# Performance work log

Hardware: AMD Instinct MI355X
Metric: run time of the kernel (lower is better)

The kernel has to match this reference:

```python
import jax, jax.numpy as jnp
import numpy as np

N = 1_048_576      # flattened batch (forward reshapes to (-1, 4))
Q_DIM = 4
HIDDEN = 64
DC = Q_DIM // 2    # q_dim_changed = 2
NUM_LO = (DC * DC - DC) // 2  # = 1
SLOPE = 0.01       # torch leaky_relu default negative slope


def setup_inputs() -> dict:
    key = jax.random.key(0)
    ks = jax.random.split(key, 9)
    def lin(kw, kb, fan_out, fan_in):
        bound = 1.0 / np.sqrt(fan_in)
        W = jax.random.uniform(kw, (fan_out, fan_in), jnp.float32, -bound, bound)
        b = jax.random.uniform(kb, (fan_out,), jnp.float32, -bound, bound)
        return W, b
    x = jax.random.normal(ks[0], (N, Q_DIM), jnp.float32)
    W1, b1 = lin(ks[1], ks[2], HIDDEN, Q_DIM)
    W2, b2 = lin(ks[3], ks[4], HIDDEN, HIDDEN)
    W_Ld, b_Ld = lin(ks[5], ks[6], DC, HIDDEN)
    W_Lo, b_Lo = lin(ks[7], ks[8], NUM_LO, HIDDEN)
    return {"x": x, "W1": W1, "b1": b1, "W2": W2, "b2": b2,
            "W_Ld": W_Ld, "b_Ld": b_Ld, "W_Lo": W_Lo, "b_Lo": b_Lo}


def reference(x, W1, b1, W2, b2, W_Ld, b_Ld, W_Lo, b_Lo):
    q = x.reshape(-1, Q_DIM)                      # (n, 4)
    n = q.shape[0]
    h1 = jax.nn.leaky_relu(q @ W1.T + b1, SLOPE)  # (n, 64)
    h2 = jax.nn.leaky_relu(h1 @ W2.T + b2, SLOPE) # (n, 64); dropout is eval-mode identity
    Ld = jax.nn.softplus(h2 @ W_Ld.T + b_Ld)      # (n, 2) positive diagonal
    Lo = h2 @ W_Lo.T + b_Lo                       # (n, 1) strictly-lower entries
    rows, cols = jnp.tril_indices(DC, -1)         # strictly lower triangle, row-major
    diag = jnp.arange(DC)
    L = jnp.zeros((n, DC, DC), dtype=q.dtype)
    L = L.at[:, rows, cols].set(Lo)               # scatter Lo (matches torch boolean-mask fill order)
    L = L.at[:, diag, diag].set(Ld)               # diag_embed(Ld)
    H = jnp.einsum('nij,nkj->nik', L, L) + 1e-9 * jnp.eye(DC, dtype=q.dtype)
    return H
```

## Files before the change

kernel.cpp:

```cpp
#include <hip/hip_runtime.h>


typedef __attribute__((ext_vector_type(8))) short bf16x8;
typedef __attribute__((ext_vector_type(4))) float f32x4;
typedef __attribute__((ext_vector_type(2))) float f32x2;

#define BLOCK_THREADS  256
#define GRID_BLOCKS    1280
#define ROWS_PER_GROUP 256

__device__ __forceinline__ float lrelu(float a) {
    return fmaxf(a, 0.01f * a);
}

__device__ __forceinline__ f32x2 lrelu2(f32x2 a) {
    return __builtin_elementwise_max(a, a * 0.01f);
}

__device__ __forceinline__ float softplus(float v) {
    return fmaxf(v, 0.0f) + log1pf(expf(-fabsf(v)));
}

__device__ __forceinline__ unsigned cvt_pk_bf16(float lo, float hi) {
    unsigned r;
    asm("v_cvt_pk_bf16_f32 %0, %1, %2" : "=v"(r) : "v"(lo), "v"(hi));
    return r;
}

__device__ __forceinline__ float lo_of(float v, unsigned pk, bool hi_half) {
    const float h = __uint_as_float(hi_half ? (pk & 0xFFFF0000u) : (pk << 16));
    return v - h;
}

__global__ __launch_bounds__(BLOCK_THREADS) void dln_mfma(
    const float* __restrict__ x,
    const float* __restrict__ W1,  const float* __restrict__ b1,
    const float* __restrict__ W2,  const float* __restrict__ b2,
    const float* __restrict__ WLd, const float* __restrict__ bLd,
    const float* __restrict__ WLo, const float* __restrict__ bLo,
    float* __restrict__ out, int ngroups)
{
    __shared__ __align__(16) unsigned short h1s[4][8][64][8];

    const int tid  = threadIdx.x;
    const int lane = tid & 63;
    const int wv   = tid >> 6;
    const int quad = lane >> 4;
    const int c    = lane & 15;

    int grp = blockIdx.x;
    float4 qnext = ((const float4*)x)[grp * ROWS_PER_GROUP + tid];

    bf16x8 afrag[4][2];
    f32x4 b2v[4];
#pragma unroll
    for (int mt = 0; mt < 4; ++mt) {
        const int nu = 32 * (mt >> 1) + 8 * (c >> 2) + 4 * (mt & 1) + (c & 3);
        const float* wr = W2 + nu * 64 + 8 * quad;
#pragma unroll
        for (int s = 0; s < 2; ++s) {
            const float4 f0 = *(const float4*)(wr + 32 * s);
            const float4 f1 = *(const float4*)(wr + 32 * s + 4);
            uint4 u;
            u.x = cvt_pk_bf16(f0.x, f0.y);
            u.y = cvt_pk_bf16(f0.z, f0.w);
            u.z = cvt_pk_bf16(f1.x, f1.y);
            u.w = cvt_pk_bf16(f1.z, f1.w);
            afrag[mt][s] = __builtin_bit_cast(bf16x8, u);
        }
        b2v[mt] = *(const f32x4*)(b2 + 32 * (mt >> 1) + 4 * (mt & 1) + 8 * quad);
    }

    bf16x8 hA[2][2];
    {
        const float* hw = (c == 0) ? WLd : (c == 1) ? (WLd + 64) : WLo;
#pragma unroll
        for (int s = 0; s < 2; ++s) {
            uint4 uh = make_uint4(0u, 0u, 0u, 0u);
            uint4 ul = make_uint4(0u, 0u, 0u, 0u);
            if (c < 3) {
                const float* p = hw + 32 * s + 8 * quad;
                const float4 f0 = *(const float4*)(p);
                const float4 f1 = *(const float4*)(p + 4);
                uh.x = cvt_pk_bf16(f0.x, f0.y);
                uh.y = cvt_pk_bf16(f0.z, f0.w);
                uh.z = cvt_pk_bf16(f1.x, f1.y);
                uh.w = cvt_pk_bf16(f1.z, f1.w);
                ul.x = cvt_pk_bf16(lo_of(f0.x, uh.x, false), lo_of(f0.y, uh.x, true));
                ul.y = cvt_pk_bf16(lo_of(f0.z, uh.y, false), lo_of(f0.w, uh.y, true));
                ul.z = cvt_pk_bf16(lo_of(f1.x, uh.z, false), lo_of(f1.y, uh.z, true));
                ul.w = cvt_pk_bf16(lo_of(f1.z, uh.w, false), lo_of(f1.w, uh.w, true));
            }
            hA[s][0] = __builtin_bit_cast(bf16x8, uh);
            hA[s][1] = __builtin_bit_cast(bf16x8, ul);
        }
    }
    const float bld0 = bLd[0];
    const float bld1 = bLd[1];
    const float blo0 = bLo[0];
    const f32x4 hinit = (quad == 0) ? (f32x4){bld0, bld1, blo0, 0.0f}
                                    : (f32x4){0.0f, 0.0f, 0.0f, 0.0f};

    for (; grp < ngroups; grp += (int)gridDim.x) {
        const float4 qv = qnext;
        const int gn = grp + (int)gridDim.x;
        if (gn < ngroups)
            qnext = ((const float4*)x)[gn * ROWS_PER_GROUP + tid];
        const int wbase = grp * ROWS_PER_GROUP + wv * 64;

#pragma unroll
        for (int ch = 0; ch < 8; ++ch) {
            unsigned up[4];
#pragma unroll
            for (int p = 0; p < 4; ++p) {
                float h[2];
#pragma unroll
                for (int e = 0; e < 2; ++e) {
                    const int j = ch * 8 + p * 2 + e;
                    float a = b1[j];
                    a = fmaf(qv.x, W1[4 * j + 0], a);
                    a = fmaf(qv.y, W1[4 * j + 1], a);
                    a = fmaf(qv.z, W1[4 * j + 2], a);
                    a = fmaf(qv.w, W1[4 * j + 3], a);
                    h[e] = lrelu(a);
                }
                up[p] = cvt_pk_bf16(h[0], h[1]);
            }
            *(uint4*)&h1s[wv][ch][lane][0] = make_uint4(up[0], up[1], up[2], up[3]);
        }

#pragma unroll
        for (int it = 0; it < 4; ++it) {
            const bf16x8 bf0 = *(const bf16x8*)&h1s[wv][quad][it * 16 + c][0];
            const bf16x8 bf1 = *(const bf16x8*)&h1s[wv][4 + quad][it * 16 + c][0];

            uint4 u0, u1;
#pragma unroll
            for (int mt = 0; mt < 4; ++mt) {
                f32x4 acc = b2v[mt];
                acc = __builtin_amdgcn_mfma_f32_16x16x32_bf16(afrag[mt][0], bf0, acc, 0, 0, 0);
                acc = __builtin_amdgcn_mfma_f32_16x16x32_bf16(afrag[mt][1], bf1, acc, 0, 0, 0);
                const f32x2 hlo = lrelu2((f32x2){acc[0], acc[1]});
                const f32x2 hhi = lrelu2((f32x2){acc[2], acc[3]});
                const unsigned pa = cvt_pk_bf16(hlo[0], hlo[1]);
                const unsigned pb = cvt_pk_bf16(hhi[0], hhi[1]);
                if (mt == 0)      { u0.x = pa; u0.y = pb; }
                else if (mt == 1) { u0.z = pa; u0.w = pb; }
                else if (mt == 2) { u1.x = pa; u1.y = pb; }
                else              { u1.z = pa; u1.w = pb; }
            }
            const bf16x8 bh0 = __builtin_bit_cast(bf16x8, u0);
            const bf16x8 bh1 = __builtin_bit_cast(bf16x8, u1);

            f32x4 hacc = hinit;
            hacc = __builtin_amdgcn_mfma_f32_16x16x32_bf16(hA[0][0], bh0, hacc, 0, 0, 0);
            hacc = __builtin_amdgcn_mfma_f32_16x16x32_bf16(hA[0][1], bh0, hacc, 0, 0, 0);
            hacc = __builtin_amdgcn_mfma_f32_16x16x32_bf16(hA[1][0], bh1, hacc, 0, 0, 0);
            hacc = __builtin_amdgcn_mfma_f32_16x16x32_bf16(hA[1][1], bh1, hacc, 0, 0, 0);

            if (quad == 0) {
                const float ld0 = softplus(hacc[0]);
                const float ld1 = softplus(hacc[1]);
                const float lo  = hacc[2];
                float4 o;
                o.x = fmaf(ld0, ld0, 1e-9f);
                o.y = ld0 * lo;
                o.z = o.y;
                o.w = fmaf(lo, lo, fmaf(ld1, ld1, 1e-9f));
                reinterpret_cast<float4*>(out)[wbase + it * 16 + c] = o;
            }
        }
    }
}

__global__ __launch_bounds__(256) void dln_tail(
    const float* __restrict__ x,
    const float* __restrict__ W1,  const float* __restrict__ b1,
    const float* __restrict__ W2,  const float* __restrict__ b2,
    const float* __restrict__ WLd, const float* __restrict__ bLd,
    const float* __restrict__ WLo, const float* __restrict__ bLo,
    float* __restrict__ out, int row0, int nrows)
{
    const int row = row0 + blockIdx.x * 256 + threadIdx.x;
    if (row >= nrows) return;
    const float4 qv = reinterpret_cast<const float4*>(x)[row];
    float h1[64];
#pragma unroll
    for (int j = 0; j < 64; ++j) {
        float a = b1[j];
        a = fmaf(qv.x, W1[4 * j + 0], a);
        a = fmaf(qv.y, W1[4 * j + 1], a);
        a = fmaf(qv.z, W1[4 * j + 2], a);
        a = fmaf(qv.w, W1[4 * j + 3], a);
        h1[j] = lrelu(a);
    }
    float ld0 = bLd[0], ld1 = bLd[1], lo = bLo[0];
#pragma unroll 4
    for (int j = 0; j < 64; ++j) {
        float a0 = b2[j], a1 = 0.0f;
        const float* w = W2 + 64 * j;
#pragma unroll
        for (int k = 0; k < 64; k += 2) {
            a0 = fmaf(h1[k],     w[k],     a0);
            a1 = fmaf(h1[k + 1], w[k + 1], a1);
        }
        const float a = lrelu(a0 + a1);
        ld0 = fmaf(a, WLd[j],      ld0);
        ld1 = fmaf(a, WLd[64 + j], ld1);
        lo  = fmaf(a, WLo[j],      lo);
    }
    ld0 = softplus(ld0);
    ld1 = softplus(ld1);
    float4 o;
    o.x = fmaf(ld0, ld0, 1e-9f);
    o.y = ld0 * lo;
    o.z = o.y;
    o.w = fmaf(lo, lo, fmaf(ld1, ld1, 1e-9f));
    reinterpret_cast<float4*>(out)[row] = o;
}

extern "C" void kernel_launch(void* const* d_in, const int* in_sizes, int n_in,
                              void* d_out, int out_size, void* d_ws, size_t ws_size,
                              hipStream_t stream)
{
    const float* x   = (const float*)d_in[0];
    const float* W1  = (const float*)d_in[1];
    const float* b1  = (const float*)d_in[2];
    const float* W2  = (const float*)d_in[3];
    const float* b2  = (const float*)d_in[4];
    const float* WLd = (const float*)d_in[5];
    const float* bLd = (const float*)d_in[6];
    const float* WLo = (const float*)d_in[7];
    const float* bLo = (const float*)d_in[8];
    float* out = (float*)d_out;

    const int nrows   = in_sizes[0] / 4;
    const int ngroups = nrows / ROWS_PER_GROUP;
    const int nfull   = ngroups * ROWS_PER_GROUP;
    const int rem     = nrows - nfull;

    if (ngroups > 0) {
        const int grid = (ngroups < GRID_BLOCKS) ? ngroups : GRID_BLOCKS;
        dln_mfma<<<grid, BLOCK_THREADS, 0, stream>>>(
            x, W1, b1, W2, b2, WLd, bLd, WLo, bLo, out, ngroups);
    }
    if (rem > 0)
        dln_tail<<<(rem + 255) / 256, 256, 0, stream>>>(
            x, W1, b1, W2, b2, WLd, bLd, WLo, bLo, out, nfull, nrows);
}
```

Before: 137.5 us.

## Compute first layer with MFMA and drop shared-memory staging and persistent loop

Moves the 4->64 first layer from per-thread scalar FMAs (staged through LDS) onto a bf16 MFMA, using hi/lo bf16 splitting of W1 and x plus a ones column to fold in the bias. The first-layer result stays in registers as the B operand of the second-layer MFMA, so the LDS buffer is removed. The persistent grid-stride loop with x prefetch is replaced by one block per 256-row group, and the final head accumulates into two independent accumulators to shorten the MFMA dependency chain. Per-block setup (weight fragment conversion) now repeats for every group instead of being amortized across a persistent block, and bf16 precision of the first layer changes slightly.

After: 147.5 us. 7.3% more time.

```diff
diff --git a/kernel.cpp b/kernel.cpp
--- a/kernel.cpp
+++ b/kernel.cpp
@@ -6,7 +6,6 @@
 typedef __attribute__((ext_vector_type(2))) float f32x2;
 
 #define BLOCK_THREADS  256
-#define GRID_BLOCKS    1280
 #define ROWS_PER_GROUP 256
 
 __device__ __forceinline__ float lrelu(float a) {
@@ -38,18 +37,42 @@
     const float* __restrict__ W2,  const float* __restrict__ b2,
     const float* __restrict__ WLd, const float* __restrict__ bLd,
     const float* __restrict__ WLo, const float* __restrict__ bLo,
-    float* __restrict__ out, int ngroups)
+    float* __restrict__ out)
 {
-    __shared__ __align__(16) unsigned short h1s[4][8][64][8];
-
     const int tid  = threadIdx.x;
     const int lane = tid & 63;
     const int wv   = tid >> 6;
     const int quad = lane >> 4;
     const int c    = lane & 15;
 
-    int grp = blockIdx.x;
-    float4 qnext = ((const float4*)x)[grp * ROWS_PER_GROUP + tid];
+    const int wbase = blockIdx.x * ROWS_PER_GROUP + wv * 64;
+
+    float4 xv[4];
+#pragma unroll
+    for (int it = 0; it < 4; ++it)
+        xv[it] = ((const float4*)x)[wbase + it * 16 + c];
+
+    bf16x8 a1[4];
+#pragma unroll
+    for (int mt = 0; mt < 4; ++mt) {
+        const int nu = 32 * (mt >> 1) + 8 * (c >> 2) + 4 * (mt & 1) + (c & 3);
+        const float4 w = *(const float4*)(W1 + 4 * nu);
+        const float bb = b1[nu];
+        const unsigned h01 = cvt_pk_bf16(w.x, w.y);
+        const unsigned h23 = cvt_pk_bf16(w.z, w.w);
+        uint4 u = make_uint4(0u, 0u, 0u, 0u);
+        if (quad == 0) {
+            const unsigned t = cvt_pk_bf16(bb, 0.0f);
+            const float bl = bb - __uint_as_float(t << 16);
+            u.x = h01; u.y = h23;
+            u.z = cvt_pk_bf16(bb, bl);
+        } else if (quad == 1) {
+            u.x = cvt_pk_bf16(lo_of(w.x, h01, false), lo_of(w.y, h01, true));
+            u.y = cvt_pk_bf16(lo_of(w.z, h23, false), lo_of(w.w, h23, true));
+            u.z = h01; u.w = h23;
+        }
+        a1[mt] = __builtin_bit_cast(bf16x8, u);
+    }
 
     bf16x8 afrag[4][2];
     f32x4 b2v[4];
@@ -95,80 +118,87 @@
             hA[s][1] = __builtin_bit_cast(bf16x8, ul);
         }
     }
-    const float bld0 = bLd[0];
-    const float bld1 = bLd[1];
-    const float blo0 = bLo[0];
-    const f32x4 hinit = (quad == 0) ? (f32x4){bld0, bld1, blo0, 0.0f}
-                                    : (f32x4){0.0f, 0.0f, 0.0f, 0.0f};
-
-    for (; grp < ngroups; grp += (int)gridDim.x) {
-        const float4 qv = qnext;
-        const int gn = grp + (int)gridDim.x;
-        if (gn < ngroups)
-            qnext = ((const float4*)x)[gn * ROWS_PER_GROUP + tid];
-        const int wbase = grp * ROWS_PER_GROUP + wv * 64;
-
-#pragma unroll
-        for (int ch = 0; ch < 8; ++ch) {
-            unsigned up[4];
-#pragma unroll
-            for (int p = 0; p < 4; ++p) {
-                float h[2];
-#pragma unroll
-                for (int e = 0; e < 2; ++e) {
-                    const int j = ch * 8 + p * 2 + e;
-                    float a = b1[j];
-                    a = fmaf(qv.x, W1[4 * j + 0], a);
-                    a = fmaf(qv.y, W1[4 * j + 1], a);
-                    a = fmaf(qv.z, W1[4 * j + 2], a);
-                    a = fmaf(qv.w, W1[4 * j + 3], a);
-                    h[e] = lrelu(a);
-                }
-                up[p] = cvt_pk_bf16(h[0], h[1]);
-            }
-            *(uint4*)&h1s[wv][ch][lane][0] = make_uint4(up[0], up[1], up[2], up[3]);
-        }
-
-#pragma unroll
-        for (int it = 0; it < 4; ++it) {
-            const bf16x8 bf0 = *(const bf16x8*)&h1s[wv][quad][it * 16 + c][0];
-            const bf16x8 bf1 = *(const bf16x8*)&h1s[wv][4 + quad][it * 16 + c][0];
-
-            uint4 u0, u1;
-#pragma unroll
-            for (int mt = 0; mt < 4; ++mt) {
-                f32x4 acc = b2v[mt];
-                acc = __builtin_amdgcn_mfma_f32_16x16x32_bf16(afrag[mt][0], bf0, acc, 0, 0, 0);
-                acc = __builtin_amdgcn_mfma_f32_16x16x32_bf16(afrag[mt][1], bf1, acc, 0, 0, 0);
-                const f32x2 hlo = lrelu2((f32x2){acc[0], acc[1]});
-                const f32x2 hhi = lrelu2((f32x2){acc[2], acc[3]});
-                const unsigned pa = cvt_pk_bf16(hlo[0], hlo[1]);
-                const unsigned pb = cvt_pk_bf16(hhi[0], hhi[1]);
-                if (mt == 0)      { u0.x = pa; u0.y = pb; }
-                else if (mt == 1) { u0.z = pa; u0.w = pb; }
-                else if (mt == 2) { u1.x = pa; u1.y = pb; }
-                else              { u1.z = pa; u1.w = pb; }
-            }
-            const bf16x8 bh0 = __builtin_bit_cast(bf16x8, u0);
-            const bf16x8 bh1 = __builtin_bit_cast(bf16x8, u1);
-
-            f32x4 hacc = hinit;
-            hacc = __builtin_amdgcn_mfma_f32_16x16x32_bf16(hA[0][0], bh0, hacc, 0, 0, 0);
-            hacc = __builtin_amdgcn_mfma_f32_16x16x32_bf16(hA[0][1], bh0, hacc, 0, 0, 0);
-            hacc = __builtin_amdgcn_mfma_f32_16x16x32_bf16(hA[1][0], bh1, hacc, 0, 0, 0);
-            hacc = __builtin_amdgcn_mfma_f32_16x16x32_bf16(hA[1][1], bh1, hacc, 0, 0, 0);
-
-            if (quad == 0) {
-                const float ld0 = softplus(hacc[0]);
-                const float ld1 = softplus(hacc[1]);
-                const float lo  = hacc[2];
-                float4 o;
-                o.x = fmaf(ld0, ld0, 1e-9f);
-                o.y = ld0 * lo;
-                o.z = o.y;
-                o.w = fmaf(lo, lo, fmaf(ld1, ld1, 1e-9f));
-                reinterpret_cast<float4*>(out)[wbase + it * 16 + c] = o;
-            }
+    const f32x4 hinit = (quad == 0)
+        ? (f32x4){bLd[0], bLd[1], bLo[0], 0.0f}
+        : (f32x4){0.0f, 0.0f, 0.0f, 0.0f};
+
+#pragma unroll
+    for (int it = 0; it < 4; ++it) {
+        const unsigned xh01 = cvt_pk_bf16(xv[it].x, xv[it].y);
+        const unsigned xh23 = cvt_pk_bf16(xv[it].z, xv[it].w);
+        uint4 ub = make_uint4(0u, 0u, 0u, 0u);
+        if (quad == 0) {
+            ub.x = xh01; ub.y = xh23; ub.z = 0x3F803F80u;
+        } else if (quad == 1) {
+            ub.x = xh01; ub.y = xh23;
+            ub.z = cvt_pk_bf16(lo_of(xv[it].x, xh01, false), lo_of(xv[it].y, xh01, true));
+            ub.w = cvt_pk_bf16(lo_of(xv[it].z, xh23, false), lo_of(xv[it].w, xh23, true));
+        }
+        const bf16x8 bx = __builtin_bit_cast(bf16x8, ub);
+
+        f32x4 acc1[4];
+#pragma unroll
+        for (int mt = 0; mt < 4; ++mt)
+            acc1[mt] = __builtin_amdgcn_mfma_f32_16x16x32_bf16(
+                a1[mt], bx, (f32x4){0.0f, 0.0f, 0.0f, 0.0f}, 0, 0, 0);
+
+        uint4 u0, u1;
+        {
+            const f32x2 p0 = lrelu2((f32x2){acc1[0][0], acc1[0][1]});
+            const f32x2 p1 = lrelu2((f32x2){acc1[0][2], acc1[0][3]});
+            const f32x2 p2 = lrelu2((f32x2){acc1[1][0], acc1[1][1]});
+            const f32x2 p3 = lrelu2((f32x2){acc1[1][2], acc1[1][3]});
+            const f32x2 p4 = lrelu2((f32x2){acc1[2][0], acc1[2][1]});
+            const f32x2 p5 = lrelu2((f32x2){acc1[2][2], acc1[2][3]});
+            const f32x2 p6 = lrelu2((f32x2){acc1[3][0], acc1[3][1]});
+            const f32x2 p7 = lrelu2((f32x2){acc1[3][2], acc1[3][3]});
+            u0.x = cvt_pk_bf16(p0[0], p0[1]);
+            u0.y = cvt_pk_bf16(p1[0], p1[1]);
+            u0.z = cvt_pk_bf16(p2[0], p2[1]);
+            u0.w = cvt_pk_bf16(p3[0], p3[1]);
+            u1.x = cvt_pk_bf16(p4[0], p4[1]);
+            u1.y = cvt_pk_bf16(p5[0], p5[1]);
+            u1.z = cvt_pk_bf16(p6[0], p6[1]);
+            u1.w = cvt_pk_bf16(p7[0], p7[1]);
+        }
+        const bf16x8 bf0 = __builtin_bit_cast(bf16x8, u0);
+        const bf16x8 bf1 = __builtin_bit_cast(bf16x8, u1);
+
+        uint4 v0, v1;
+#pragma unroll
+        for (int mt = 0; mt < 4; ++mt) {
+            f32x4 acc = b2v[mt];
+            acc = __builtin_amdgcn_mfma_f32_16x16x32_bf16(afrag[mt][0], bf0, acc, 0, 0, 0);
+            acc = __builtin_amdgcn_mfma_f32_16x16x32_bf16(afrag[mt][1], bf1, acc, 0, 0, 0);
+            const f32x2 hlo = lrelu2((f32x2){acc[0], acc[1]});
+            const f32x2 hhi = lrelu2((f32x2){acc[2], acc[3]});
+            const unsigned pa = cvt_pk_bf16(hlo[0], hlo[1]);
+            const unsigned pb = cvt_pk_bf16(hhi[0], hhi[1]);
+            if (mt == 0)      { v0.x = pa; v0.y = pb; }
+            else if (mt == 1) { v0.z = pa; v0.w = pb; }
+            else if (mt == 2) { v1.x = pa; v1.y = pb; }
+            else              { v1.z = pa; v1.w = pb; }
+        }
+        const bf16x8 bh0 = __builtin_bit_cast(bf16x8, v0);
+        const bf16x8 bh1 = __builtin_bit_cast(bf16x8, v1);
+
+        f32x4 ha = hinit;
+        f32x4 hb = (f32x4){0.0f, 0.0f, 0.0f, 0.0f};
+        ha = __builtin_amdgcn_mfma_f32_16x16x32_bf16(hA[0][0], bh0, ha, 0, 0, 0);
+        hb = __builtin_amdgcn_mfma_f32_16x16x32_bf16(hA[0][1], bh0, hb, 0, 0, 0);
+        ha = __builtin_amdgcn_mfma_f32_16x16x32_bf16(hA[1][0], bh1, ha, 0, 0, 0);
+        hb = __builtin_amdgcn_mfma_f32_16x16x32_bf16(hA[1][1], bh1, hb, 0, 0, 0);
+
+        if (quad == 0) {
+            const float ld0 = softplus(ha[0] + hb[0]);
+            const float ld1 = softplus(ha[1] + hb[1]);
+            const float lo  = ha[2] + hb[2];
+            float4 o;
+            o.x = fmaf(ld0, ld0, 1e-9f);
+            o.y = ld0 * lo;
+            o.z = o.y;
+            o.w = fmaf(lo, lo, fmaf(ld1, ld1, 1e-9f));
+            reinterpret_cast<float4*>(out)[wbase + it * 16 + c] = o;
         }
     }
 }
@@ -239,11 +269,9 @@
     const int nfull   = ngroups * ROWS_PER_GROUP;
     const int rem     = nrows - nfull;
 
-    if (ngroups > 0) {
-        const int grid = (ngroups < GRID_BLOCKS) ? ngroups : GRID_BLOCKS;
-        dln_mfma<<<grid, BLOCK_THREADS, 0, stream>>>(
-            x, W1, b1, W2, b2, WLd, bLd, WLo, bLo, out, ngroups);
-    }
+    if (ngroups > 0)
+        dln_mfma<<<ngroups, BLOCK_THREADS, 0, stream>>>(
+            x, W1, b1, W2, b2, WLd, bLd, WLo, bLo, out);
     if (rem > 0)
         dln_tail<<<(rem + 255) / 256, 256, 0, stream>>>(
             x, W1, b1, W2, b2, WLd, bLd, WLo, bLo, out, nfull, nrows);
```
